# Performance work log

Measured on AMD Instinct MI355X. Metric: run time of the kernel, lower is better.

The kernel has to match this reference:

```python
import jax, jax.numpy as jnp
import numpy as np

N_NODES = 50000
N_EDGES = 800000
IN_DIM = 128
HID_DIM = 128


def _gcn_norm(edge_index, num_nodes):
    # Add self-loops, then symmetric normalization D^-1/2 (A+I) D^-1/2
    loop = jnp.arange(num_nodes, dtype=edge_index.dtype)
    row = jnp.concatenate([edge_index[0], loop])  # source nodes
    col = jnp.concatenate([edge_index[1], loop])  # target nodes
    ew = jnp.ones(row.shape[0], dtype=jnp.float32)
    deg = jax.ops.segment_sum(ew, col, num_segments=num_nodes)
    dinv = jnp.where(deg > 0, jax.lax.rsqrt(deg), 0.0)
    norm = dinv[row] * ew * dinv[col]
    return row, col, norm


def _gcn_layer(h, row, col, norm, W, b, num_nodes):
    h = h @ W                              # [N, D] linear transform first
    msg = h[row] * norm[:, None]           # gather + normalize  [E+N, D]
    out = jax.ops.segment_sum(msg, col, num_segments=num_nodes)  # scatter-add
    return out + b


def setup_inputs() -> dict:
    key = jax.random.key(0)
    k1, k2, k3, k4 = jax.random.split(key, 4)
    x = jax.random.normal(k1, (N_NODES, IN_DIM), dtype=jnp.float32)
    edge_index = jax.random.randint(k2, (2, N_EDGES), 0, N_NODES, dtype=jnp.int32)
    W1 = jax.random.normal(k3, (IN_DIM, HID_DIM), dtype=jnp.float32) * (1.0 / np.sqrt(IN_DIM))
    b1 = jnp.zeros((HID_DIM,), dtype=jnp.float32)
    W2 = jax.random.normal(k4, (HID_DIM, HID_DIM), dtype=jnp.float32) * (1.0 / np.sqrt(HID_DIM))
    b2 = jnp.zeros((HID_DIM,), dtype=jnp.float32)
    return {"x": x, "edge_index": edge_index, "W1": W1, "b1": b1, "W2": W2, "b2": b2}


def reference(x, edge_index, W1, b1, W2, b2):
    n = x.shape[0]
    row, col, norm = _gcn_norm(edge_index, n)
    z = _gcn_layer(x, row, col, norm, W1, b1, n)
    z = jax.nn.relu(z)
    z = _gcn_layer(z, row, col, norm, W2, b2, n)
    z = jax.nn.relu(z)
    return z
```

## Files before the change

### kernel.cpp

```cpp
#include <hip/hip_runtime.h>
#include <hip/hip_bf16.h>
#include <hip/hip_fp16.h>


#define BK 128
#define CAP 4096
#define PACK_ROWBITS 20
#define NB_MAX 512
#define CHUNK 2048

typedef __attribute__((ext_vector_type(4))) _Float16 f16x4;
typedef __attribute__((ext_vector_type(4))) float f32x4;

__global__ __launch_bounds__(256) void k_fused(const int* __restrict__ row,
                                               const int* __restrict__ col,
                                               int* gcur, unsigned* ebuf,
                                               int E, int nb,
                                               const float* __restrict__ A,
                                               const float* __restrict__ W,
                                               __half* __restrict__ C, int M,
                                               int nScat) {
    __shared__ union {
        struct { int h[NB_MAX]; int base[NB_MAX]; } sc;
        _Float16 Wt[128][136];
    } u;
    const int t = threadIdx.x;

    if (blockIdx.x < nScat) {
        const int e0 = blockIdx.x * CHUNK;
        int cs[CHUNK / 256];
        for (int i = t; i < nb; i += 256) u.sc.h[i] = 0;
        __syncthreads();
#pragma unroll
        for (int q = 0; q < CHUNK / 256; q++) {
            int e = e0 + q * 256 + t;
            cs[q] = (e < E) ? col[e] : -1;
            if (cs[q] >= 0) atomicAdd(&u.sc.h[cs[q] >> 7], 1);
        }
        __syncthreads();
        for (int i = t; i < nb; i += 256) {
            u.sc.base[i] = u.sc.h[i] ? atomicAdd(&gcur[i], u.sc.h[i]) : 0;
            u.sc.h[i] = 0;
        }
        __syncthreads();
#pragma unroll
        for (int q = 0; q < CHUNK / 256; q++) {
            int e = e0 + q * 256 + t;
            if (cs[q] >= 0) {
                int c = cs[q];
                int b = c >> 7;
                int loc = atomicAdd(&u.sc.h[b], 1);
                ebuf[b * CAP + u.sc.base[b] + loc] =
                    (unsigned)row[e] | ((unsigned)(c & (BK - 1)) << PACK_ROWBITS);
            }
        }
    } else {
        const int bid = blockIdx.x - nScat;
        for (int idx = t; idx < 4096; idx += 256) {
            int k = idx >> 5, n4 = (idx & 31) << 2;
            float4 w4 = ((const float4*)W)[idx];
            u.Wt[n4 + 0][k] = (_Float16)w4.x;
            u.Wt[n4 + 1][k] = (_Float16)w4.y;
            u.Wt[n4 + 2][k] = (_Float16)w4.z;
            u.Wt[n4 + 3][k] = (_Float16)w4.w;
        }
        __syncthreads();

        const int wave = t >> 6, lane = t & 63;
        const int l16 = lane & 15, g = lane >> 4;
        const int rbase = bid * 64 + wave * 16;
        int r = rbase + l16;
        if (r >= M) r = M - 1;

        f32x4 acc[8];
#pragma unroll
        for (int ct = 0; ct < 8; ct++) acc[ct] = (f32x4){0.f, 0.f, 0.f, 0.f};

#pragma unroll
        for (int s = 0; s < 8; s++) {
            const int k0 = s * 16 + g * 4;
            float4 a4 = *(const float4*)(A + (size_t)r * 128 + k0);
            f16x4 a = (f16x4){(_Float16)a4.x, (_Float16)a4.y,
                              (_Float16)a4.z, (_Float16)a4.w};
#pragma unroll
            for (int ct = 0; ct < 8; ct++) {
                f16x4 b = *(const f16x4*)(&u.Wt[ct * 16 + l16][k0]);
                acc[ct] = __builtin_amdgcn_mfma_f32_16x16x16f16(a, b, acc[ct], 0, 0, 0);
            }
        }

#pragma unroll
        for (int ct = 0; ct < 8; ct++) {
#pragma unroll
            for (int i = 0; i < 4; i++) {
                int rr = rbase + g * 4 + i;
                if (rr < M)
                    C[(size_t)rr * 128 + ct * 16 + l16] = __float2half(acc[ct][i]);
            }
        }
    }
}

__global__ __launch_bounds__(1024) void k_bnodefill(const unsigned* __restrict__ ebuf,
                                                    const int* __restrict__ gcur,
                                                    int* degi, float* dinv, int* startv,
                                                    int* srcs, int N) {
    __shared__ int h[BK];
    __shared__ int sc[BK];
    const int t = threadIdx.x, b = blockIdx.x;
    const int s = b * CAP;
    const int cnt = gcur[b];
    if (t < BK) h[t] = 0;
    __syncthreads();
    for (int i = t; i < cnt; i += 1024)
        atomicAdd(&h[(ebuf[s + i] >> PACK_ROWBITS) & (BK - 1)], 1);
    __syncthreads();
    int deg = (t < BK) ? h[t] : 0;
    if (t < BK) sc[t] = deg;
    __syncthreads();
    for (int o = 1; o < BK; o <<= 1) {
        int x = (t < BK && t >= o) ? sc[t - o] : 0;
        __syncthreads();
        if (t < BK) sc[t] += x;
        __syncthreads();
    }
    int node = b * BK + t;
    if (t < BK) {
        int lexcl = sc[t] - deg;
        if (node < N) {
            degi[node]   = deg;
            dinv[node]   = rsqrtf((float)deg + 1.0f);
            startv[node] = s + lexcl;
        }
        h[t] = lexcl;
    }
    __syncthreads();
    for (int i = t; i < cnt; i += 1024) {
        unsigned u = ebuf[s + i];
        int c = (u >> PACK_ROWBITS) & (BK - 1);
        int loc = atomicAdd(&h[c], 1);
        srcs[s + loc] = (int)(u & ((1u << PACK_ROWBITS) - 1));
    }
}

__global__ __launch_bounds__(256) void k_gemm2(const __half* __restrict__ A,
                                               const float* __restrict__ W,
                                               __half* __restrict__ C, int M) {
    __shared__ _Float16 Wt[128][136];
    const int t = threadIdx.x;
    for (int idx = t; idx < 4096; idx += 256) {
        int k = idx >> 5, n4 = (idx & 31) << 2;
        float4 w4 = ((const float4*)W)[idx];
        Wt[n4 + 0][k] = (_Float16)w4.x;
        Wt[n4 + 1][k] = (_Float16)w4.y;
        Wt[n4 + 2][k] = (_Float16)w4.z;
        Wt[n4 + 3][k] = (_Float16)w4.w;
    }
    __syncthreads();

    const int wave = t >> 6, lane = t & 63;
    const int l16 = lane & 15, g = lane >> 4;
    const int rbase = blockIdx.x * 64 + wave * 16;
    int r = rbase + l16;
    if (r >= M) r = M - 1;

    f32x4 acc[8];
#pragma unroll
    for (int ct = 0; ct < 8; ct++) acc[ct] = (f32x4){0.f, 0.f, 0.f, 0.f};

#pragma unroll
    for (int s = 0; s < 8; s++) {
        const int k0 = s * 16 + g * 4;
        f16x4 a = *(const f16x4*)((const _Float16*)A + (size_t)r * 128 + k0);
#pragma unroll
        for (int ct = 0; ct < 8; ct++) {
            f16x4 b = *(const f16x4*)(&Wt[ct * 16 + l16][k0]);
            acc[ct] = __builtin_amdgcn_mfma_f32_16x16x16f16(a, b, acc[ct], 0, 0, 0);
        }
    }

#pragma unroll
    for (int ct = 0; ct < 8; ct++) {
#pragma unroll
        for (int i = 0; i < 4; i++) {
            int rr = rbase + g * 4 + i;
            if (rr < M)
                C[(size_t)rr * 128 + ct * 16 + l16] = __float2half(acc[ct][i]);
        }
    }
}

__global__ __launch_bounds__(256) void k_agg(const __half* __restrict__ H,
                                             const int* __restrict__ srcs,
                                             const int* __restrict__ startv,
                                             const int* __restrict__ degi,
                                             const float* __restrict__ dinv,
                                             const float* __restrict__ bias,
                                             float* __restrict__ outF,
                                             __half* __restrict__ outH, int n) {
    int wave = threadIdx.x >> 6, lane = threadIdx.x & 63;
    int node = blockIdx.x * 4 + wave;
    if (node >= n) return;
    int s0 = startv[node];
    int d = degi[node];
    float di = dinv[node];
    const __half2* Hv = (const __half2*)H;

    float2 hv = __half22float2(Hv[(size_t)node * 64 + lane]);
    float ax = di * hv.x, ay = di * hv.y;

    for (int k = 0; k < d; k += 64) {
        int take = d - k; if (take > 64) take = 64;
        int idx = (lane < take) ? srcs[s0 + k + lane] : node;
        float djl = (lane < take) ? dinv[idx] : 0.f;
        for (int u = 0; u < take; u += 16) {
            int jj[16]; __half2 hh[16];
#pragma unroll
            for (int q = 0; q < 16; q++)
                jj[q] = __shfl(idx, u + q);
#pragma unroll
            for (int q = 0; q < 16; q++)
                hh[q] = Hv[(size_t)jj[q] * 64 + lane];
#pragma unroll
            for (int q = 0; q < 16; q++) {
                float dj = __shfl(djl, u + q);
                float2 v = __half22float2(hh[q]);
                ax = fmaf(dj, v.x, ax);
                ay = fmaf(dj, v.y, ay);
            }
        }
    }
    float2 b2 = ((const float2*)bias)[lane];
    float ox = fmaxf(fmaf(di, ax, b2.x), 0.f);
    float oy = fmaxf(fmaf(di, ay, b2.y), 0.f);
    if (outF) {
        ((float2*)outF)[(size_t)node * 64 + lane] = make_float2(ox, oy);
    } else {
        __half2 p = __floats2half2_rn(ox, oy);
        ((__half2*)outH)[(size_t)node * 64 + lane] = p;
    }
}

extern "C" void kernel_launch(void* const* d_in, const int* in_sizes, int n_in,
                              void* d_out, int out_size, void* d_ws, size_t ws_size,
                              hipStream_t stream) {
    const float* x  = (const float*)d_in[0];
    const int*   ei = (const int*)d_in[1];
    const float* W1 = (const float*)d_in[2];
    const float* b1 = (const float*)d_in[3];
    const float* W2 = (const float*)d_in[4];
    const float* b2 = (const float*)d_in[5];
    const int N = in_sizes[0] / 128;
    const int E = in_sizes[1] / 2;
    const int NB = (N + BK - 1) / BK;

    char* w = (char*)d_ws;
    auto alloc = [&](size_t bytes) -> void* {
        void* p = (void*)w;
        w += (bytes + 255) & ~(size_t)255;
        return p;
    };
    int*      degi     = (int*)alloc((size_t)N * 4);
    float*    dinv     = (float*)alloc((size_t)N * 4);
    int*      startv   = (int*)alloc((size_t)N * 4);
    int*      gcur     = (int*)alloc((size_t)NB * 4);
    unsigned* ebuf     = (unsigned*)alloc((size_t)NB * CAP * 4);
    int*      srcs     = (int*)alloc((size_t)NB * CAP * 4);
    __half*   H        = (__half*)alloc((size_t)N * 128 * 2);
    __half*   Z        = (__half*)alloc((size_t)N * 128 * 2);

    const int* rowp = ei;
    const int* colp = ei + E;
    const int nScat = (E + CHUNK - 1) / CHUNK;
    const int nGemm = (N + 63) / 64;

    (void)hipMemsetAsync(gcur, 0, (size_t)NB * 4, stream);
    k_fused<<<nScat + nGemm, 256, 0, stream>>>(rowp, colp, gcur, ebuf, E, NB,
                                               x, W1, H, N, nScat);
    k_bnodefill<<<NB, 1024, 0, stream>>>(ebuf, gcur, degi, dinv, startv, srcs, N);

    k_agg<<<(N + 3) / 4, 256, 0, stream>>>(H, srcs, startv, degi, dinv, b1,
                                           nullptr, Z, N);
    k_gemm2<<<nGemm, 256, 0, stream>>>(Z, W2, H, N);
    k_agg<<<(N + 3) / 4, 256, 0, stream>>>(H, srcs, startv, degi, dinv, b2,
                                           (float*)d_out, nullptr, N);
}
```

Before: 144.5 us.

## Fuse layer-1 aggregation with layer-2 GEMM and pretranspose W2 once

```diff
diff --git a/kernel.cpp b/kernel.cpp
--- a/kernel.cpp
+++ b/kernel.cpp
@@ -104,10 +104,19 @@
 __global__ __launch_bounds__(1024) void k_bnodefill(const unsigned* __restrict__ ebuf,
                                                     const int* __restrict__ gcur,
                                                     int* degi, float* dinv, int* startv,
-                                                    int* srcs, int N) {
+                                                    int* srcs, int N,
+                                                    const float* __restrict__ W2,
+                                                    _Float16* __restrict__ W2t, int NB) {
+    const int t = threadIdx.x, b = blockIdx.x;
+    if (b == NB) {
+        for (int idx = t; idx < 16384; idx += 1024) {
+            int k = idx >> 7, nn = idx & 127;
+            W2t[nn * 128 + k] = (_Float16)W2[k * 128 + nn];
+        }
+        return;
+    }
     __shared__ int h[BK];
     __shared__ int sc[BK];
-    const int t = threadIdx.x, b = blockIdx.x;
     const int s = b * CAP;
     const int cnt = gcur[b];
     if (t < BK) h[t] = 0;
@@ -143,27 +152,59 @@
     }
 }
 
-__global__ __launch_bounds__(256) void k_gemm2(const __half* __restrict__ A,
-                                               const float* __restrict__ W,
-                                               __half* __restrict__ C, int M) {
-    __shared__ _Float16 Wt[128][136];
+__global__ __launch_bounds__(256) void k_aggemm(const __half* __restrict__ H,
+                                                const int* __restrict__ srcs,
+                                                const int* __restrict__ startv,
+                                                const int* __restrict__ degi,
+                                                const float* __restrict__ dinv,
+                                                const float* __restrict__ bias,
+                                                const _Float16* __restrict__ W2t,
+                                                __half* __restrict__ Hout, int n) {
+    __shared__ _Float16 Zl[64][136];
     const int t = threadIdx.x;
-    for (int idx = t; idx < 4096; idx += 256) {
-        int k = idx >> 5, n4 = (idx & 31) << 2;
-        float4 w4 = ((const float4*)W)[idx];
-        Wt[n4 + 0][k] = (_Float16)w4.x;
-        Wt[n4 + 1][k] = (_Float16)w4.y;
-        Wt[n4 + 2][k] = (_Float16)w4.z;
-        Wt[n4 + 3][k] = (_Float16)w4.w;
-    }
-    __syncthreads();
-
     const int wave = t >> 6, lane = t & 63;
+    const int nodeBase = blockIdx.x * 64 + wave * 16;
+    const __half2* Hv = (const __half2*)H;
+    const float2 b2 = ((const float2*)bias)[lane];
+
+    for (int i = 0; i < 16; i++) {
+        int node = nodeBase + i;
+        int nodec = (node < n) ? node : (n - 1);
+        int s0 = startv[nodec];
+        int d = degi[nodec];
+        float di = dinv[nodec];
+        float2 hv = __half22float2(Hv[(size_t)nodec * 64 + lane]);
+        float ax = di * hv.x, ay = di * hv.y;
+
+        for (int k = 0; k < d; k += 64) {
+            int take = d - k; if (take > 64) take = 64;
+            int idx = (lane < take) ? srcs[s0 + k + lane] : nodec;
+            float djl = (lane < take) ? dinv[idx] : 0.f;
+            for (int u = 0; u < take; u += 16) {
+                int jj[16]; __half2 hh[16];
+#pragma unroll
+                for (int q = 0; q < 16; q++)
+                    jj[q] = __shfl(idx, u + q);
+#pragma unroll
+                for (int q = 0; q < 16; q++)
+                    hh[q] = Hv[(size_t)jj[q] * 64 + lane];
+#pragma unroll
+                for (int q = 0; q < 16; q++) {
+                    float dj = __shfl(djl, u + q);
+                    float2 v = __half22float2(hh[q]);
+                    ax = fmaf(dj, v.x, ax);
+                    ay = fmaf(dj, v.y, ay);
+                }
+            }
+        }
+        float ox = fmaxf(fmaf(di, ax, b2.x), 0.f);
+        float oy = fmaxf(fmaf(di, ay, b2.y), 0.f);
+        __half2 p = __floats2half2_rn(ox, oy);
+        *(__half2*)(&Zl[wave * 16 + i][2 * lane]) = p;
+    }
+    __syncthreads();
+
     const int l16 = lane & 15, g = lane >> 4;
-    const int rbase = blockIdx.x * 64 + wave * 16;
-    int r = rbase + l16;
-    if (r >= M) r = M - 1;
-
     f32x4 acc[8];
 #pragma unroll
     for (int ct = 0; ct < 8; ct++) acc[ct] = (f32x4){0.f, 0.f, 0.f, 0.f};
@@ -171,10 +212,10 @@
 #pragma unroll
     for (int s = 0; s < 8; s++) {
         const int k0 = s * 16 + g * 4;
-        f16x4 a = *(const f16x4*)((const _Float16*)A + (size_t)r * 128 + k0);
+        f16x4 a = *(const f16x4*)(&Zl[wave * 16 + l16][k0]);
 #pragma unroll
         for (int ct = 0; ct < 8; ct++) {
-            f16x4 b = *(const f16x4*)(&Wt[ct * 16 + l16][k0]);
+            f16x4 b = *(const f16x4*)(W2t + (ct * 16 + l16) * 128 + k0);
             acc[ct] = __builtin_amdgcn_mfma_f32_16x16x16f16(a, b, acc[ct], 0, 0, 0);
         }
     }
@@ -183,9 +224,9 @@
     for (int ct = 0; ct < 8; ct++) {
 #pragma unroll
         for (int i = 0; i < 4; i++) {
-            int rr = rbase + g * 4 + i;
-            if (rr < M)
-                C[(size_t)rr * 128 + ct * 16 + l16] = __float2half(acc[ct][i]);
+            int rr = nodeBase + g * 4 + i;
+            if (rr < n)
+                Hout[(size_t)rr * 128 + ct * 16 + l16] = __float2half(acc[ct][i]);
         }
     }
 }
@@ -196,8 +237,7 @@
                                              const int* __restrict__ degi,
                                              const float* __restrict__ dinv,
                                              const float* __restrict__ bias,
-                                             float* __restrict__ outF,
-                                             __half* __restrict__ outH, int n) {
+                                             float* __restrict__ out, int n) {
     int wave = threadIdx.x >> 6, lane = threadIdx.x & 63;
     int node = blockIdx.x * 4 + wave;
     if (node >= n) return;
@@ -233,12 +273,7 @@
     float2 b2 = ((const float2*)bias)[lane];
     float ox = fmaxf(fmaf(di, ax, b2.x), 0.f);
     float oy = fmaxf(fmaf(di, ay, b2.y), 0.f);
-    if (outF) {
-        ((float2*)outF)[(size_t)node * 64 + lane] = make_float2(ox, oy);
-    } else {
-        __half2 p = __floats2half2_rn(ox, oy);
-        ((__half2*)outH)[(size_t)node * 64 + lane] = p;
-    }
+    ((float2*)out)[(size_t)node * 64 + lane] = make_float2(ox, oy);
 }
 
 extern "C" void kernel_launch(void* const* d_in, const int* in_sizes, int n_in,
@@ -267,7 +302,8 @@
     unsigned* ebuf     = (unsigned*)alloc((size_t)NB * CAP * 4);
     int*      srcs     = (int*)alloc((size_t)NB * CAP * 4);
     __half*   H        = (__half*)alloc((size_t)N * 128 * 2);
-    __half*   Z        = (__half*)alloc((size_t)N * 128 * 2);
+    __half*   H2       = (__half*)alloc((size_t)N * 128 * 2);
+    _Float16* W2t      = (_Float16*)alloc((size_t)128 * 128 * 2);
 
     const int* rowp = ei;
     const int* colp = ei + E;
@@ -277,11 +313,9 @@
     (void)hipMemsetAsync(gcur, 0, (size_t)NB * 4, stream);
     k_fused<<<nScat + nGemm, 256, 0, stream>>>(rowp, colp, gcur, ebuf, E, NB,
                                                x, W1, H, N, nScat);
-    k_bnodefill<<<NB, 1024, 0, stream>>>(ebuf, gcur, degi, dinv, startv, srcs, N);
-
-    k_agg<<<(N + 3) / 4, 256, 0, stream>>>(H, srcs, startv, degi, dinv, b1,
-                                           nullptr, Z, N);
-    k_gemm2<<<nGemm, 256, 0, stream>>>(Z, W2, H, N);
-    k_agg<<<(N + 3) / 4, 256, 0, stream>>>(H, srcs, startv, degi, dinv, b2,
-                                           (float*)d_out, nullptr, N);
-}
+    k_bnodefill<<<NB + 1, 1024, 0, stream>>>(ebuf, gcur, degi, dinv, startv, srcs, N,
+                                             W2, W2t, NB);
+    k_aggemm<<<nGemm, 256, 0, stream>>>(H, srcs, startv, degi, dinv, b1, W2t, H2, N);
+    k_agg<<<(N + 3) / 4, 256, 0, stream>>>(H2, srcs, startv, degi, dinv, b2,
+                                           (float*)d_out, N);
+}
```

Measured after the change: 187.8 us. +29.9%, slower.
